# Performance work log

Measured on AMD Instinct MI355X. Metric: run time of the kernel, lower is better.

## Reference

```python
import jax, jax.numpy as jnp
import numpy as np
import math

NUM_HEADS = 8
QUERY_SIZE = 256
QK_SIZE = QUERY_SIZE // NUM_HEADS  # 32
VO_SIZE = QUERY_SIZE // NUM_HEADS  # 32
SEQ = 4096


def setup_inputs() -> dict:
    key = jax.random.key(0)
    kq, kk, kv, km, kwq, kwk, kwv, kwo = jax.random.split(key, 8)
    # equinox Linear weight shape is (out_features, in_features); y = W @ x
    lim_in = 1.0 / math.sqrt(QUERY_SIZE)
    lim_hd = 1.0 / math.sqrt(NUM_HEADS * VO_SIZE)
    return {
        "query": jax.random.normal(kq, (SEQ, QUERY_SIZE), dtype=jnp.float32),
        "key_": jax.random.normal(kk, (SEQ, QUERY_SIZE), dtype=jnp.float32),
        "value": jax.random.normal(kv, (SEQ, QUERY_SIZE), dtype=jnp.float32),
        "radial_mask": jax.random.uniform(km, (SEQ,), dtype=jnp.float32),
        "Wq": jax.random.uniform(kwq, (NUM_HEADS * QK_SIZE, QUERY_SIZE), minval=-lim_in, maxval=lim_in, dtype=jnp.float32),
        "Wk": jax.random.uniform(kwk, (NUM_HEADS * QK_SIZE, QUERY_SIZE), minval=-lim_in, maxval=lim_in, dtype=jnp.float32),
        "Wv": jax.random.uniform(kwv, (NUM_HEADS * VO_SIZE, QUERY_SIZE), minval=-lim_in, maxval=lim_in, dtype=jnp.float32),
        "Wo": jax.random.uniform(kwo, (QUERY_SIZE, NUM_HEADS * VO_SIZE), minval=-lim_hd, maxval=lim_hd, dtype=jnp.float32),
    }


def reference(query, key_, value, radial_mask, Wq, Wk, Wv, Wo):
    S = query.shape[0]
    # QKV projections, split into heads: [S, H, D]
    q = (query @ Wq.T).reshape(S, NUM_HEADS, QK_SIZE)
    k = (key_ @ Wk.T).reshape(S, NUM_HEADS, QK_SIZE)
    v = (value @ Wv.T).reshape(S, NUM_HEADS, VO_SIZE)
    # radial scaling of values (per kv position)
    v = radial_mask[:, None, None] * v
    # scaled dot-product attention per head; logits: [H, S, S]
    scale = 1.0 / math.sqrt(QK_SIZE)
    logits = jnp.einsum("shd,Shd->hsS", q * scale, k)
    weights = jax.nn.softmax(logits, axis=-1)
    attn = jnp.einsum("hsS,Shd->shd", weights, v).reshape(S, NUM_HEADS * VO_SIZE)
    # output projection
    return attn @ Wo.T
```

## Files before the change

kernel.cpp:

```cpp
#include <hip/hip_runtime.h>
#include <cstdint>

#define SEQ 4096
#define NH 8
#define DH 32

typedef __bf16 bf16x8 __attribute__((ext_vector_type(8)));
typedef float f32x4 __attribute__((ext_vector_type(4)));
typedef float f32x8 __attribute__((ext_vector_type(8)));
typedef float f32x16 __attribute__((ext_vector_type(16)));
typedef unsigned short u16x8 __attribute__((ext_vector_type(8)));
typedef unsigned u32x4 __attribute__((ext_vector_type(4)));
typedef unsigned u32x2 __attribute__((ext_vector_type(2)));
typedef int i32x2 __attribute__((ext_vector_type(2)));

#define MFMA16 __builtin_amdgcn_mfma_f32_16x16x32_bf16
#define MFMA32 __builtin_amdgcn_mfma_f32_32x32x16_bf16

#define QSCALE 0.25503902427f

__device__ inline bf16x8 ld_bf8(const unsigned short* p) {
    return __builtin_bit_cast(bf16x8, *(const u16x8*)p);
}
__device__ inline unsigned short bfbits(float v) {
    return __builtin_bit_cast(unsigned short, (__bf16)v);
}
__device__ inline bf16x8 cvt_f8(f32x8 v) {
    bf16x8 r;
#pragma unroll
    for (int i = 0; i < 8; i++) r[i] = (__bf16)v[i];
    return r;
}
__device__ inline unsigned cvtpk(float lo, float hi) {
    unsigned r;
    asm("v_cvt_pk_bf16_f32 %0, %1, %2" : "=v"(r) : "v"(lo), "v"(hi));
    return r;
}

__global__ __launch_bounds__(256) void precvt_kernel(
    const float* __restrict__ x0, const float* __restrict__ x1, const float* __restrict__ x2,
    const float* __restrict__ w0, const float* __restrict__ w1, const float* __restrict__ w2,
    const float* __restrict__ w3,
    unsigned short* __restrict__ bx0, unsigned short* __restrict__ bx1,
    unsigned short* __restrict__ bx2, unsigned short* __restrict__ bw0,
    unsigned short* __restrict__ bw1, unsigned short* __restrict__ bw2,
    unsigned short* __restrict__ bw3) {
    const int i = blockIdx.x * 256 + threadIdx.x;
    const float* src;
    unsigned short* dst;
    int off;
    float scale = 1.0f;
    if (i < 393216) {
        const int sel = i >> 17;
        off = i & 131071;
        src = (sel == 0) ? x0 : (sel == 1) ? x1 : x2;
        dst = (sel == 0) ? bx0 : (sel == 1) ? bx1 : bx2;
        if (sel == 0) scale = QSCALE;
    } else {
        const int j = i - 393216;
        const int sel = j >> 13;
        off = j & 8191;
        src = (sel == 0) ? w0 : (sel == 1) ? w1 : (sel == 2) ? w2 : w3;
        dst = (sel == 0) ? bw0 : (sel == 1) ? bw1 : (sel == 2) ? bw2 : bw3;
    }
    f32x8 v = ((const f32x8*)src)[off];
    u16x8 r;
#pragma unroll
    for (int j = 0; j < 8; j++) r[j] = bfbits(v[j] * scale);
    ((u16x8*)dst)[off] = r;
}

__global__ __launch_bounds__(256, 4) void proj_bf16_kernel(
    const unsigned short* __restrict__ X0, const unsigned short* __restrict__ X1,
    const unsigned short* __restrict__ X2, const unsigned short* __restrict__ W0,
    const unsigned short* __restrict__ W1, const unsigned short* __restrict__ W2,
    const float* __restrict__ radial,
    unsigned short* __restrict__ outq, unsigned short* __restrict__ outk,
    unsigned short* __restrict__ outv) {
    const int sel = blockIdx.y;
    const unsigned short* X = (sel == 0) ? X0 : (sel == 1) ? X1 : X2;
    const unsigned short* W = (sel == 0) ? W0 : (sel == 1) ? W1 : W2;
    const int lane = threadIdx.x & 63;
    const int w = threadIdx.x >> 6;
    const int cl = lane & 15;
    const int h4 = lane >> 4;
    const int t = blockIdx.x * 4 + w;
    const int m0 = (t >> 3) * 32;
    const int n0 = (t & 7) * 32;

    const unsigned short* xa0 = X + (m0 + cl) * 256 + h4 * 8;
    const unsigned short* xa1 = xa0 + 16 * 256;
    const unsigned short* wb0 = W + (n0 + cl) * 256 + h4 * 8;
    const unsigned short* wb1 = wb0 + 16 * 256;

    f32x4 acc00 = {0.f, 0.f, 0.f, 0.f}, acc01 = {0.f, 0.f, 0.f, 0.f};
    f32x4 acc10 = {0.f, 0.f, 0.f, 0.f}, acc11 = {0.f, 0.f, 0.f, 0.f};

    if (sel < 2) {
#pragma unroll
        for (int ksi = 0; ksi < 8; ksi++) {
            bf16x8 a0 = ld_bf8(xa0 + ksi * 32);
            bf16x8 a1 = ld_bf8(xa1 + ksi * 32);
            bf16x8 b0 = ld_bf8(wb0 + ksi * 32);
            bf16x8 b1 = ld_bf8(wb1 + ksi * 32);
            acc00 = MFMA16(a0, b0, acc00, 0, 0, 0);
            acc01 = MFMA16(a0, b1, acc01, 0, 0, 0);
            acc10 = MFMA16(a1, b0, acc10, 0, 0, 0);
            acc11 = MFMA16(a1, b1, acc11, 0, 0, 0);
        }
        unsigned short* out = (sel == 0) ? outq : outk;
#pragma unroll
        for (int am = 0; am < 2; am++) {
#pragma unroll
            for (int r = 0; r < 4; r++) {
                const int cm = m0 + am * 16 + h4 * 4 + r;
#pragma unroll
                for (int bn = 0; bn < 2; bn++) {
                    float v = am ? (bn ? acc11[r] : acc10[r]) : (bn ? acc01[r] : acc00[r]);
                    const int cn = n0 + bn * 16 + cl;
                    const int h = cn >> 5, d = cn & 31;
                    out[(h * SEQ + cm) * DH + d] = bfbits(v);
                }
            }
        }
    } else {
#pragma unroll
        for (int ksi = 0; ksi < 8; ksi++) {
            bf16x8 a0 = ld_bf8(xa0 + ksi * 32);
            bf16x8 a1 = ld_bf8(xa1 + ksi * 32);
            bf16x8 b0 = ld_bf8(wb0 + ksi * 32);
            bf16x8 b1 = ld_bf8(wb1 + ksi * 32);
            acc00 = MFMA16(b0, a0, acc00, 0, 0, 0);
            acc01 = MFMA16(b0, a1, acc01, 0, 0, 0);
            acc10 = MFMA16(b1, a0, acc10, 0, 0, 0);
            acc11 = MFMA16(b1, a1, acc11, 0, 0, 0);
        }
        const int h = n0 >> 5;
        const float rm0 = radial[m0 + cl];
        const float rm1 = radial[m0 + 16 + cl];
#pragma unroll
        for (int wb = 0; wb < 2; wb++) {
#pragma unroll
            for (int r = 0; r < 4; r++) {
                const int d = wb * 16 + h4 * 4 + r;
                unsigned short* vrow = outv + (h * DH + d) * SEQ + m0;
                float v0 = wb ? acc10[r] : acc00[r];
                float v1 = wb ? acc11[r] : acc01[r];
                vrow[cl] = bfbits(v0 * rm0);
                vrow[16 + cl] = bfbits(v1 * rm1);
            }
        }
    }
}

__global__ __launch_bounds__(256) void proj_f32_kernel(
    const float* __restrict__ X0, const float* __restrict__ X1, const float* __restrict__ X2,
    const float* __restrict__ W0, const float* __restrict__ W1, const float* __restrict__ W2,
    const float* __restrict__ radial,
    unsigned short* __restrict__ outq, unsigned short* __restrict__ outk,
    unsigned short* __restrict__ outv) {
    const int sel = blockIdx.y;
    const float* X = (sel == 0) ? X0 : (sel == 1) ? X1 : X2;
    const float* W = (sel == 0) ? W0 : (sel == 1) ? W1 : W2;
    const int lane = threadIdx.x & 63;
    const int w = threadIdx.x >> 6;
    const int cl = lane & 15;
    const int h4 = lane >> 4;
    const int t = blockIdx.x * 4 + w;
    const int m0 = (t >> 3) * 32;
    const int n0 = (t & 7) * 32;

    const float* xa0 = X + (m0 + cl) * 256 + h4 * 8;
    const float* xa1 = xa0 + 16 * 256;
    const float* wb0 = W + (n0 + cl) * 256 + h4 * 8;
    const float* wb1 = wb0 + 16 * 256;

    f32x4 acc00 = {0.f, 0.f, 0.f, 0.f}, acc01 = {0.f, 0.f, 0.f, 0.f};
    f32x4 acc10 = {0.f, 0.f, 0.f, 0.f}, acc11 = {0.f, 0.f, 0.f, 0.f};
    if (sel < 2) {
#pragma unroll
        for (int ksi = 0; ksi < 8; ksi++) {
            bf16x8 a0 = cvt_f8(*(const f32x8*)(xa0 + ksi * 32));
            bf16x8 a1 = cvt_f8(*(const f32x8*)(xa1 + ksi * 32));
            bf16x8 b0 = cvt_f8(*(const f32x8*)(wb0 + ksi * 32));
            bf16x8 b1 = cvt_f8(*(const f32x8*)(wb1 + ksi * 32));
            acc00 = MFMA16(a0, b0, acc00, 0, 0, 0);
            acc01 = MFMA16(a0, b1, acc01, 0, 0, 0);
            acc10 = MFMA16(a1, b0, acc10, 0, 0, 0);
            acc11 = MFMA16(a1, b1, acc11, 0, 0, 0);
        }
        const float qs = (sel == 0) ? QSCALE : 1.0f;
        unsigned short* out = (sel == 0) ? outq : outk;
#pragma unroll
        for (int am = 0; am < 2; am++) {
#pragma unroll
            for (int r = 0; r < 4; r++) {
                const int cm = m0 + am * 16 + h4 * 4 + r;
#pragma unroll
                for (int bn = 0; bn < 2; bn++) {
                    float v = am ? (bn ? acc11[r] : acc10[r]) : (bn ? acc01[r] : acc00[r]);
                    const int cn = n0 + bn * 16 + cl;
                    const int h = cn >> 5, d = cn & 31;
                    out[(h * SEQ + cm) * DH + d] = bfbits(v * qs);
                }
            }
        }
    } else {
#pragma unroll
        for (int ksi = 0; ksi < 8; ksi++) {
            bf16x8 a0 = cvt_f8(*(const f32x8*)(xa0 + ksi * 32));
            bf16x8 a1 = cvt_f8(*(const f32x8*)(xa1 + ksi * 32));
            bf16x8 b0 = cvt_f8(*(const f32x8*)(wb0 + ksi * 32));
            bf16x8 b1 = cvt_f8(*(const f32x8*)(wb1 + ksi * 32));
            acc00 = MFMA16(b0, a0, acc00, 0, 0, 0);
            acc01 = MFMA16(b0, a1, acc01, 0, 0, 0);
            acc10 = MFMA16(b1, a0, acc10, 0, 0, 0);
            acc11 = MFMA16(b1, a1, acc11, 0, 0, 0);
        }
        const int h = n0 >> 5;
        const float rm0 = radial[m0 + cl];
        const float rm1 = radial[m0 + 16 + cl];
#pragma unroll
        for (int wb = 0; wb < 2; wb++) {
#pragma unroll
            for (int r = 0; r < 4; r++) {
                const int d = wb * 16 + h4 * 4 + r;
                unsigned short* vrow = outv + (h * DH + d) * SEQ + m0;
                float v0 = wb ? acc10[r] : acc00[r];
                float v1 = wb ? acc11[r] : acc01[r];
                vrow[cl] = bfbits(v0 * rm0);
                vrow[16 + cl] = bfbits(v1 * rm1);
            }
        }
    }
}

__device__ inline f32x16 qk_step(bf16x8 kf0, bf16x8 kf1, const bf16x8& qf0,
                                 const bf16x8& qf1) {
    f32x16 s = {0.f, 0.f, 0.f, 0.f, 0.f, 0.f, 0.f, 0.f,
                0.f, 0.f, 0.f, 0.f, 0.f, 0.f, 0.f, 0.f};
    s = MFMA32(kf0, qf0, s, 0, 0, 0);
    s = MFMA32(kf1, qf1, s, 0, 0, 0);
    return s;
}

__device__ inline void sm_pv_step(const f32x16& s, bf16x8 vt0, bf16x8 vt1,
                                  f32x16& oacc, float& ls) {
    float p[16];
#pragma unroll
    for (int r = 0; r < 16; r++) p[r] = __builtin_amdgcn_exp2f(s[r]);
    {
        float s01 = p[0] + p[1], s23 = p[2] + p[3], s45 = p[4] + p[5], s67 = p[6] + p[7];
        float s89 = p[8] + p[9], sab = p[10] + p[11], scd = p[12] + p[13], sef = p[14] + p[15];
        ls += ((s01 + s23) + (s45 + s67)) + ((s89 + sab) + (scd + sef));
    }
    unsigned a01 = cvtpk(p[0], p[1]), a23 = cvtpk(p[2], p[3]);
    unsigned a45 = cvtpk(p[4], p[5]), a67 = cvtpk(p[6], p[7]);
    i32x2 r0 = __builtin_amdgcn_permlane32_swap((int)a01, (int)a45, false, false);
    i32x2 r1 = __builtin_amdgcn_permlane32_swap((int)a23, (int)a67, false, false);
    u32x4 pb0w = {(unsigned)r0[0], (unsigned)r1[0], (unsigned)r0[1], (unsigned)r1[1]};
    unsigned a89 = cvtpk(p[8], p[9]), aab = cvtpk(p[10], p[11]);
    unsigned acd = cvtpk(p[12], p[13]), aef = cvtpk(p[14], p[15]);
    i32x2 r2 = __builtin_amdgcn_permlane32_swap((int)a89, (int)acd, false, false);
    i32x2 r3 = __builtin_amdgcn_permlane32_swap((int)aab, (int)aef, false, false);
    u32x4 pb1w = {(unsigned)r2[0], (unsigned)r3[0], (unsigned)r2[1], (unsigned)r3[1]};
    oacc = MFMA32(vt0, __builtin_bit_cast(bf16x8, pb0w), oacc, 0, 0, 0);
    oacc = MFMA32(vt1, __builtin_bit_cast(bf16x8, pb1w), oacc, 0, 0, 0);
}

__global__ __launch_bounds__(512, 2) __attribute__((amdgpu_waves_per_eu(2, 2)))
void attn_kernel(
    const unsigned short* __restrict__ Q, const unsigned short* __restrict__ K,
    const unsigned short* __restrict__ Vt, unsigned short* __restrict__ An) {
    __shared__ float cO[7][64][16];
    __shared__ float cls[7][4][32];
    const int lane = threadIdx.x & 63;
    const int w = threadIdx.x >> 6;
    const int l31 = lane & 31;
    const int hi = lane >> 5;

    int bid = blockIdx.x;
    bid = (bid & 7) * 32 + (bid >> 3);
    const int head = bid >> 5;
    const int m0 = (bid & 31) * 128;

    const unsigned short* qh = Q + head * (SEQ * DH);
    const unsigned short* kh = K + head * (SEQ * DH);
    const unsigned short* vh = Vt + head * (DH * SEQ);

    bf16x8 q0[4], q1[4];
#pragma unroll
    for (int c = 0; c < 4; c++) {
        q0[c] = ld_bf8(qh + (m0 + c * 32 + l31) * DH + hi * 8);
        q1[c] = ld_bf8(qh + (m0 + c * 32 + l31) * DH + 16 + hi * 8);
    }

    f32x16 o[4];
    float ls[4];
#pragma unroll
    for (int c = 0; c < 4; c++) {
        o[c] = (f32x16){0.f, 0.f, 0.f, 0.f, 0.f, 0.f, 0.f, 0.f,
                        0.f, 0.f, 0.f, 0.f, 0.f, 0.f, 0.f, 0.f};
        ls[c] = 0.f;
    }

    const unsigned short* kp = kh + (w * 512 + l31) * DH + hi * 8;
    const unsigned short* vp = vh + l31 * SEQ + w * 512 + hi * 8;

    bf16x8 kc0 = ld_bf8(kp), kc1 = ld_bf8(kp + 16);
    bf16x8 vo0 = ld_bf8(vp), vo1 = ld_bf8(vp + 16);
    f32x16 so0 = qk_step(kc0, kc1, q0[0], q1[0]);
    f32x16 so1 = qk_step(kc0, kc1, q0[1], q1[1]);
    f32x16 so2 = qk_step(kc0, kc1, q0[2], q1[2]);
    f32x16 so3 = qk_step(kc0, kc1, q0[3], q1[3]);

    for (int nb = 0; nb < 15; nb++) {
        kp += 32 * DH;
        vp += 32;
        bf16x8 kn0 = ld_bf8(kp), kn1 = ld_bf8(kp + 16);
        bf16x8 vn0 = ld_bf8(vp), vn1 = ld_bf8(vp + 16);
        sm_pv_step(so0, vo0, vo1, o[0], ls[0]);
        f32x16 sn0 = qk_step(kn0, kn1, q0[0], q1[0]);
        sm_pv_step(so1, vo0, vo1, o[1], ls[1]);
        f32x16 sn1 = qk_step(kn0, kn1, q0[1], q1[1]);
        sm_pv_step(so2, vo0, vo1, o[2], ls[2]);
        f32x16 sn2 = qk_step(kn0, kn1, q0[2], q1[2]);
        sm_pv_step(so3, vo0, vo1, o[3], ls[3]);
        f32x16 sn3 = qk_step(kn0, kn1, q0[3], q1[3]);
        so0 = sn0; so1 = sn1; so2 = sn2; so3 = sn3;
        vo0 = vn0; vo1 = vn1;
    }
    sm_pv_step(so0, vo0, vo1, o[0], ls[0]);
    sm_pv_step(so1, vo0, vo1, o[1], ls[1]);
    sm_pv_step(so2, vo0, vo1, o[2], ls[2]);
    sm_pv_step(so3, vo0, vo1, o[3], ls[3]);

#pragma unroll
    for (int c = 0; c < 4; c++) ls[c] += __shfl_xor(ls[c], 32);

#pragma unroll
    for (int c = 0; c < 4; c++) {
        if (w > 0) {
#pragma unroll
            for (int i = 0; i < 16; i++) cO[w - 1][lane][i] = o[c][i];
            if (hi == 0) cls[w - 1][c][l31] = ls[c];
        }
        __syncthreads();
        if (w == 0) {
#pragma unroll
            for (int j = 0; j < 7; j++) {
#pragma unroll
                for (int i = 0; i < 16; i++) o[c][i] += cO[j][lane][i];
            }
        }
        __syncthreads();
    }

    if (w == 0) {
#pragma unroll
        for (int c = 0; c < 4; c++) {
            float lt = ls[c];
#pragma unroll
            for (int j = 0; j < 7; j++) lt += cls[j][c][l31];
            const float inv = 1.0f / lt;
            unsigned short* op = An + (m0 + c * 32 + l31) * 256 + head * DH;
#pragma unroll
            for (int g = 0; g < 4; g++) {
                unsigned lo = cvtpk(o[c][4 * g] * inv, o[c][4 * g + 1] * inv);
                unsigned hw = cvtpk(o[c][4 * g + 2] * inv, o[c][4 * g + 3] * inv);
                *(u32x2*)(op + 8 * g + 4 * hi) = (u32x2){lo, hw};
            }
        }
    }
}

__global__ __launch_bounds__(256, 4) void oproj_bf16_kernel(
    const unsigned short* __restrict__ An, const unsigned short* __restrict__ Wo,
    float* __restrict__ out) {
    const int lane = threadIdx.x & 63;
    const int w = threadIdx.x >> 6;
    const int cl = lane & 15;
    const int h4 = lane >> 4;
    const int t = blockIdx.x * 4 + w;
    const int m0 = (t >> 4) * 32;
    const int n0 = (t & 15) * 16;

    const unsigned short* ap0 = An + (m0 + cl) * 256 + h4 * 8;
    const unsigned short* ap1 = ap0 + 16 * 256;
    const unsigned short* wb0 = Wo + (n0 + cl) * 256 + h4 * 8;

    f32x4 acc00 = {0.f, 0.f, 0.f, 0.f}, acc10 = {0.f, 0.f, 0.f, 0.f};
#pragma unroll
    for (int ksi = 0; ksi < 8; ksi++) {
        bf16x8 a0 = ld_bf8(ap0 + ksi * 32);
        bf16x8 a1 = ld_bf8(ap1 + ksi * 32);
        bf16x8 b0 = ld_bf8(wb0 + ksi * 32);
        acc00 = MFMA16(a0, b0, acc00, 0, 0, 0);
        acc10 = MFMA16(a1, b0, acc10, 0, 0, 0);
    }
#pragma unroll
    for (int am = 0; am < 2; am++) {
#pragma unroll
        for (int r = 0; r < 4; r++) {
            const int cm = m0 + am * 16 + h4 * 4 + r;
            out[cm * 256 + n0 + cl] = am ? acc10[r] : acc00[r];
        }
    }
}

__global__ __launch_bounds__(256) void oproj_f32_kernel(
    const unsigned short* __restrict__ An, const float* __restrict__ Wo,
    float* __restrict__ out) {
    const int lane = threadIdx.x & 63;
    const int w = threadIdx.x >> 6;
    const int cl = lane & 15;
    const int h4 = lane >> 4;
    const int t = blockIdx.x * 4 + w;
    const int m0 = (t >> 3) * 32;
    const int n0 = (t & 7) * 32;

    const unsigned short* ap0 = An + (m0 + cl) * 256 + h4 * 8;
    const unsigned short* ap1 = ap0 + 16 * 256;
    const float* wb0 = Wo + (n0 + cl) * 256 + h4 * 8;
    const float* wb1 = wb0 + 16 * 256;

    f32x4 acc00 = {0.f, 0.f, 0.f, 0.f}, acc01 = {0.f, 0.f, 0.f, 0.f};
    f32x4 acc10 = {0.f, 0.f, 0.f, 0.f}, acc11 = {0.f, 0.f, 0.f, 0.f};
#pragma unroll
    for (int ksi = 0; ksi < 8; ksi++) {
        bf16x8 a0 = ld_bf8(ap0 + ksi * 32);
        bf16x8 a1 = ld_bf8(ap1 + ksi * 32);
        bf16x8 b0 = cvt_f8(*(const f32x8*)(wb0 + ksi * 32));
        bf16x8 b1 = cvt_f8(*(const f32x8*)(wb1 + ksi * 32));
        acc00 = MFMA16(a0, b0, acc00, 0, 0, 0);
        acc01 = MFMA16(a0, b1, acc01, 0, 0, 0);
        acc10 = MFMA16(a1, b0, acc10, 0, 0, 0);
        acc11 = MFMA16(a1, b1, acc11, 0, 0, 0);
    }
#pragma unroll
    for (int am = 0; am < 2; am++) {
#pragma unroll
        for (int r = 0; r < 4; r++) {
            const int cm = m0 + am * 16 + h4 * 4 + r;
#pragma unroll
            for (int bn = 0; bn < 2; bn++) {
                float v = am ? (bn ? acc11[r] : acc10[r]) : (bn ? acc01[r] : acc00[r]);
                out[cm * 256 + n0 + bn * 16 + cl] = v;
            }
        }
    }
}

extern "C" void kernel_launch(void* const* d_in, const int* in_sizes, int n_in,
                              void* d_out, int out_size, void* d_ws, size_t ws_size,
                              hipStream_t stream) {
    const float* query = (const float*)d_in[0];
    const float* key_ = (const float*)d_in[1];
    const float* value = (const float*)d_in[2];
    const float* radial = (const float*)d_in[3];
    const float* Wq = (const float*)d_in[4];
    const float* Wk = (const float*)d_in[5];
    const float* Wv = (const float*)d_in[6];
    const float* Wo = (const float*)d_in[7];

    const size_t MB = 1u << 20;
    uint8_t* base = (uint8_t*)d_ws;
    unsigned short* wq = (unsigned short*)(base + 0 * MB);
    unsigned short* wk = (unsigned short*)(base + 2 * MB);
    unsigned short* wv = (unsigned short*)(base + 4 * MB);
    unsigned short* wa = (unsigned short*)(base + 6 * MB);

    if (ws_size >= (size_t)(15.5 * 1024 * 1024)) {
        unsigned short* bX0 = (unsigned short*)(base + 8 * MB);
        unsigned short* bX1 = (unsigned short*)(base + 10 * MB);
        unsigned short* bX2 = (unsigned short*)(base + 12 * MB);
        unsigned short* bWq = (unsigned short*)(base + 14 * MB);
        unsigned short* bWk = (unsigned short*)(base + 14 * MB + 128 * 1024);
        unsigned short* bWv = (unsigned short*)(base + 14 * MB + 256 * 1024);
        unsigned short* bWo = (unsigned short*)(base + 14 * MB + 384 * 1024);
        precvt_kernel<<<1664, 256, 0, stream>>>(query, key_, value, Wq, Wk, Wv, Wo,
                                                bX0, bX1, bX2, bWq, bWk, bWv, bWo);
        proj_bf16_kernel<<<dim3(256, 3), 256, 0, stream>>>(bX0, bX1, bX2, bWq, bWk, bWv,
                                                           radial, wq, wk, wv);
        attn_kernel<<<256, 512, 0, stream>>>(wq, wk, wv, wa);
        oproj_bf16_kernel<<<512, 256, 0, stream>>>(wa, bWo, (float*)d_out);
    } else {
        proj_f32_kernel<<<dim3(256, 3), 256, 0, stream>>>(query, key_, value, Wq, Wk, Wv,
                                                          radial, wq, wk, wv);
        attn_kernel<<<256, 512, 0, stream>>>(wq, wk, wv, wa);
        oproj_f32_kernel<<<256, 256, 0, stream>>>(wa, Wo, (float*)d_out);
    }
}
```

Baseline: 58.70 us.

## Prefetch K two blocks ahead and parallelize split-KV reduction across all waves

The attention main loop now keeps two K tiles in flight (loading K for block nb+2 while computing nb+1), which deepens the software pipeline to hide global-load latency. The cross-wave epilogue reduction is restructured so every wave writes its partial O and row-sum into a padded shared buffer, and then each wave reduces two output columns across all eight waves and writes them out. Previously wave 0 alone summed seven partials and did the normalization and store. The change adds register pressure from the extra K buffer, which matters under the 2-waves-per-EU bound, and adds an extra store to shared memory for wave 0.

```diff
diff --git a/kernel.cpp b/kernel.cpp
--- a/kernel.cpp
+++ b/kernel.cpp
@@ -272,8 +272,7 @@
 void attn_kernel(
     const unsigned short* __restrict__ Q, const unsigned short* __restrict__ K,
     const unsigned short* __restrict__ Vt, unsigned short* __restrict__ An) {
-    __shared__ float cO[7][64][16];
-    __shared__ float cls[7][4][32];
+    __shared__ float cO[8][64][17];
     const int lane = threadIdx.x & 63;
     const int w = threadIdx.x >> 6;
     const int l31 = lane & 31;
@@ -307,28 +306,30 @@
     const unsigned short* kp = kh + (w * 512 + l31) * DH + hi * 8;
     const unsigned short* vp = vh + l31 * SEQ + w * 512 + hi * 8;
 
-    bf16x8 kc0 = ld_bf8(kp), kc1 = ld_bf8(kp + 16);
+    bf16x8 ka0 = ld_bf8(kp), ka1 = ld_bf8(kp + 16);
     bf16x8 vo0 = ld_bf8(vp), vo1 = ld_bf8(vp + 16);
-    f32x16 so0 = qk_step(kc0, kc1, q0[0], q1[0]);
-    f32x16 so1 = qk_step(kc0, kc1, q0[1], q1[1]);
-    f32x16 so2 = qk_step(kc0, kc1, q0[2], q1[2]);
-    f32x16 so3 = qk_step(kc0, kc1, q0[3], q1[3]);
+    bf16x8 kb0 = ld_bf8(kp + 32 * DH), kb1 = ld_bf8(kp + 32 * DH + 16);
+    f32x16 so0 = qk_step(ka0, ka1, q0[0], q1[0]);
+    f32x16 so1 = qk_step(ka0, ka1, q0[1], q1[1]);
+    f32x16 so2 = qk_step(ka0, ka1, q0[2], q1[2]);
+    f32x16 so3 = qk_step(ka0, ka1, q0[3], q1[3]);
 
     for (int nb = 0; nb < 15; nb++) {
+        bf16x8 kc0 = ld_bf8(kp + 64 * DH), kc1 = ld_bf8(kp + 64 * DH + 16);
+        bf16x8 vn0 = ld_bf8(vp + 32), vn1 = ld_bf8(vp + 48);
+        sm_pv_step(so0, vo0, vo1, o[0], ls[0]);
+        f32x16 sn0 = qk_step(kb0, kb1, q0[0], q1[0]);
+        sm_pv_step(so1, vo0, vo1, o[1], ls[1]);
+        f32x16 sn1 = qk_step(kb0, kb1, q0[1], q1[1]);
+        sm_pv_step(so2, vo0, vo1, o[2], ls[2]);
+        f32x16 sn2 = qk_step(kb0, kb1, q0[2], q1[2]);
+        sm_pv_step(so3, vo0, vo1, o[3], ls[3]);
+        f32x16 sn3 = qk_step(kb0, kb1, q0[3], q1[3]);
         kp += 32 * DH;
         vp += 32;
-        bf16x8 kn0 = ld_bf8(kp), kn1 = ld_bf8(kp + 16);
-        bf16x8 vn0 = ld_bf8(vp), vn1 = ld_bf8(vp + 16);
-        sm_pv_step(so0, vo0, vo1, o[0], ls[0]);
-        f32x16 sn0 = qk_step(kn0, kn1, q0[0], q1[0]);
-        sm_pv_step(so1, vo0, vo1, o[1], ls[1]);
-        f32x16 sn1 = qk_step(kn0, kn1, q0[1], q1[1]);
-        sm_pv_step(so2, vo0, vo1, o[2], ls[2]);
-        f32x16 sn2 = qk_step(kn0, kn1, q0[2], q1[2]);
-        sm_pv_step(so3, vo0, vo1, o[3], ls[3]);
-        f32x16 sn3 = qk_step(kn0, kn1, q0[3], q1[3]);
+        kb0 = kc0; kb1 = kc1;
+        vo0 = vn0; vo1 = vn1;
         so0 = sn0; so1 = sn1; so2 = sn2; so3 = sn3;
-        vo0 = vn0; vo1 = vn1;
     }
     sm_pv_step(so0, vo0, vo1, o[0], ls[0]);
     sm_pv_step(so1, vo0, vo1, o[1], ls[1]);
@@ -338,39 +339,25 @@
 #pragma unroll
     for (int c = 0; c < 4; c++) ls[c] += __shfl_xor(ls[c], 32);
 
+    const int i0 = 2 * w;
+    const int d0 = 8 * (w >> 1) + 4 * hi + ((2 * w) & 3);
 #pragma unroll
     for (int c = 0; c < 4; c++) {
-        if (w > 0) {
-#pragma unroll
-            for (int i = 0; i < 16; i++) cO[w - 1][lane][i] = o[c][i];
-            if (hi == 0) cls[w - 1][c][l31] = ls[c];
-        }
+#pragma unroll
+        for (int i = 0; i < 16; i++) cO[w][lane][i] = o[c][i];
+        if (hi == 0) cO[w][l31][16] = ls[c];
         __syncthreads();
-        if (w == 0) {
-#pragma unroll
-            for (int j = 0; j < 7; j++) {
-#pragma unroll
-                for (int i = 0; i < 16; i++) o[c][i] += cO[j][lane][i];
-            }
-        }
+        float a = 0.f, b = 0.f, lt = 0.f;
+#pragma unroll
+        for (int j = 0; j < 8; j++) {
+            a += cO[j][lane][i0];
+            b += cO[j][lane][i0 + 1];
+            lt += cO[j][l31][16];
+        }
+        const float inv = 1.0f / lt;
+        unsigned pk = cvtpk(a * inv, b * inv);
+        *(unsigned*)(An + (m0 + c * 32 + l31) * 256 + head * DH + d0) = pk;
         __syncthreads();
-    }
-
-    if (w == 0) {
-#pragma unroll
-        for (int c = 0; c < 4; c++) {
-            float lt = ls[c];
-#pragma unroll
-            for (int j = 0; j < 7; j++) lt += cls[j][c][l31];
-            const float inv = 1.0f / lt;
-            unsigned short* op = An + (m0 + c * 32 + l31) * 256 + head * DH;
-#pragma unroll
-            for (int g = 0; g < 4; g++) {
-                unsigned lo = cvtpk(o[c][4 * g] * inv, o[c][4 * g + 1] * inv);
-                unsigned hw = cvtpk(o[c][4 * g + 2] * inv, o[c][4 * g + 3] * inv);
-                *(u32x2*)(op + 8 * g + 4 * hi) = (u32x2){lo, hw};
-            }
-        }
     }
 }
 
```

After: 58.46 us. Within noise of the previous version (-0.4%).
